# Kernel optimization log

Measured on AMD Instinct MI355X. Metric: run time of the kernel, lower is better.

The kernel has to match this reference:

```python
import jax, jax.numpy as jnp
import numpy as np

DT = 0.1
THRESH = 0.01


def setup_inputs() -> dict:
    key = jax.random.key(0)
    ks = jax.random.split(key, 4)
    B, C, H, W = 4, 64, 128, 128
    field = jax.random.normal(ks[0], (B, C, H, W), dtype=jnp.float32)
    # depthwise 3x3 conv weight [C,1,3,3], fan_in = 9
    dw = jax.random.normal(ks[1], (C, 1, 3, 3), dtype=jnp.float32) * (1.0 / 3.0)
    db = jnp.zeros((C,), jnp.float32)
    # 1x1 convs as matrices: w1 [2C, C], w2 [C, 2C]
    w1 = jax.random.normal(ks[2], (2 * C, C), dtype=jnp.float32) * (1.0 / np.sqrt(C))
    b1 = jnp.zeros((2 * C,), jnp.float32)
    w2 = jax.random.normal(ks[3], (C, 2 * C), dtype=jnp.float32) * (1.0 / np.sqrt(2 * C))
    b2 = jnp.zeros((C,), jnp.float32)
    dcoeff = jnp.ones((1,), jnp.float32) * 0.1  # diffusion_coeff init
    return {"field": field, "dw": dw, "db": db, "w1": w1, "b1": b1,
            "w2": w2, "b2": b2, "dcoeff": dcoeff, "max_steps": 50}


def _dynamics(f, dw, db, w1, b1, w2, b2, dcoeff):
    C = f.shape[1]
    diff = jax.lax.conv_general_dilated(
        f, dw, window_strides=(1, 1), padding="SAME",
        feature_group_count=C,
        dimension_numbers=("NCHW", "OIHW", "NCHW")) + db[None, :, None, None]
    h = jax.nn.gelu(jnp.einsum("bchw,oc->bohw", f, w1) + b1[None, :, None, None],
                    approximate=False)
    react = jnp.einsum("bchw,oc->bohw", h, w2) + b2[None, :, None, None]
    return dcoeff[0] * diff + react


def reference(field, dw, db, w1, b1, w2, b2, dcoeff, max_steps):
    def step(carry, _):
        f, done, steps = carry
        deriv = _dynamics(f, dw, db, w1, b1, w2, b2, dcoeff)
        new_f = f + DT * deriv
        change = jnp.mean(jnp.abs(new_f - f))
        f2 = jnp.where(done, f, new_f)          # freeze field once converged
        steps2 = steps + jnp.where(done, 0, 1)  # steps_taken is adaptive
        done2 = done | (change < THRESH)
        return (f2, done2, steps2), None

    init = (field, jnp.asarray(False), jnp.asarray(0, jnp.int32))
    (final_field, _, steps), _ = jax.lax.scan(step, init, None, length=max_steps)
    return final_field, steps
```

## Files before the change

kernel.cpp:

```cpp
#include <hip/hip_runtime.h>
#include <math.h>

#define BATCH 4
#define CCH   64
#define HDIM  128
#define WDIM  128
#define HW    (HDIM * WDIM)
#define NELEM (BATCH * CCH * HW)
#define OCH   128
#define NSTEPS 50
#define NBLK  1024
#define DT 0.1f
#define THRESH 0.01f

typedef short bf16x8 __attribute__((ext_vector_type(8)));
typedef float f32x4  __attribute__((ext_vector_type(4)));

struct Ctl {
    int done;
    int steps;
};

__global__ void init_kernel(Ctl* ctl) {
    ctl->done = 0;
    ctl->steps = 0;
}

__device__ __forceinline__ short f2bf(float x) {
    unsigned u = __float_as_uint(x);
    unsigned r = u + 0x7fff + ((u >> 16) & 1);
    return (short)(r >> 16);
}

__device__ __forceinline__ int pk(float a, float b) {
    return (f2bf(a) & 0xffff) | (((int)f2bf(b)) << 16);
}

__device__ __forceinline__ float bf_lo(int v) { return __int_as_float(v << 16); }
__device__ __forceinline__ float bf_hi(int v) { return __int_as_float(v & 0xffff0000); }

__global__ void prep_kernel(const float* __restrict__ w1,
                            const float* __restrict__ w2,
                            short* __restrict__ w1b, short* __restrict__ w2b) {
    int i = blockIdx.x * blockDim.x + threadIdx.x;
    if (i < OCH * CCH) {
        w1b[i] = f2bf(w1[i]);
        w2b[i] = f2bf(w2[i]);
    }
}

__device__ __forceinline__ float gelu_fast(float x) {
    float u  = x * 0.70710678118654752f;
    float au = fabsf(u);
    float t  = __builtin_amdgcn_rcpf(fmaf(0.3275911f, au, 1.0f));
    float p  = fmaf(1.061405429f, t, -1.453152027f);
    p = fmaf(p, t, 1.421413741f);
    p = fmaf(p, t, -0.284496736f);
    p = fmaf(p, t, 0.254829592f);
    p = p * t;
    float ex = __expf(-au * au);
    float e  = fmaf(-p, ex, 1.0f);
    float er = copysignf(e, x);
    return 0.5f * x * (1.0f + er);
}

__global__ __launch_bounds__(256, 4) void step_kernel(
    const float* __restrict__ fin, float* __restrict__ fout,
    const float* __restrict__ dw, const float* __restrict__ db,
    const short* __restrict__ w1b, const float* __restrict__ b1,
    const short* __restrict__ w2b, const float* __restrict__ b2,
    const float* __restrict__ dcoeff, const Ctl* __restrict__ ctl,
    double* __restrict__ psum)
{
    if (ctl->done) return;

    const int tid  = threadIdx.x;
    const int lane = tid & 63;
    const int w    = tid >> 6;
    const int quad = (lane >> 4);
    const int lp   = lane & 15;
    const int blk  = blockIdx.x;
    const int xcd  = blk & 7;
    const int idx  = blk >> 3;
    const int y    = xcd * 16 + (idx & 15);
    const int b    = (idx >> 4) & 3;
    const int seg  = idx >> 6;
    const int px0  = seg * 64;
    const int fbase = b * CCH * HW + y * WDIM + px0;

    __shared__ int4  sBf4[64 * 8];
    __shared__ int4  sH4 [64 * 16];
    __shared__ float sSeam[384];
    __shared__ float sDw[CCH * 9];
    __shared__ float sDb[CCH];
    __shared__ float wred[4];
    short* sBf = (short*)sBf4;
    short* sH  = (short*)sH4;
    int*   sRi = (int*)sBf4;

    for (int i = tid; i < CCH * 9; i += 256) sDw[i] = dw[i];
    if (tid < CCH) sDb[tid] = db[tid];

    if (tid < 192) {
        #pragma unroll
        for (int k = 0; k < 2; ++k) {
            int e    = tid * 2 + k;
            int row  = e >> 7;
            int side = (e >> 6) & 1;
            int ch   = e & 63;
            int gy   = y - 1 + row;
            int gx   = px0 + (side ? 64 : -1);
            float v  = 0.0f;
            if (gy >= 0 && gy < HDIM && gx >= 0 && gx < WDIM)
                v = fin[b * CCH * HW + ch * HW + gy * WDIM + gx];
            sSeam[e] = v;
        }
    }

    bf16x8 a1[2][2];
    #pragma unroll
    for (int mt = 0; mt < 2; ++mt)
        #pragma unroll
        for (int kk = 0; kk < 2; ++kk)
            a1[mt][kk] = *(const bf16x8*)(w1b + (w * 32 + mt * 16 + lp) * CCH
                                          + kk * 32 + quad * 8);
    f32x4 b1v[2];
    #pragma unroll
    for (int mt = 0; mt < 2; ++mt)
        b1v[mt] = *(const f32x4*)(b1 + w * 32 + mt * 16 + quad * 4);
    f32x4 b2v = *(const f32x4*)(b2 + w * 16 + quad * 4);

    float f[16];
    {
        #pragma unroll
        for (int i = 0; i < 16; ++i)
            f[i] = fin[fbase + (w * 16 + i) * HW + lane];
        int4 v0, v1;
        v0.x = pk(f[0], f[1]);   v0.y = pk(f[2], f[3]);
        v0.z = pk(f[4], f[5]);   v0.w = pk(f[6], f[7]);
        v1.x = pk(f[8], f[9]);   v1.y = pk(f[10], f[11]);
        v1.z = pk(f[12], f[13]); v1.w = pk(f[14], f[15]);
        int g0 = (w * 2)     ^ (lane & 7);
        int g1 = (w * 2 + 1) ^ (lane & 7);
        sBf4[lane * 8 + g0] = v0;
        sBf4[lane * 8 + g1] = v1;
    }
    __syncthreads();

    f32x4 acc1[2][4];
    #pragma unroll
    for (int mt = 0; mt < 2; ++mt)
        #pragma unroll
        for (int nt = 0; nt < 4; ++nt)
            acc1[mt][nt] = (f32x4)0.0f;

    #pragma unroll
    for (int kk = 0; kk < 2; ++kk) {
        #pragma unroll
        for (int nt = 0; nt < 4; ++nt) {
            int px = nt * 16 + lp;
            int g  = kk * 4 + quad;
            bf16x8 bfrag = *(const bf16x8*)(sBf + px * 64 + (g ^ (px & 7)) * 8);
            #pragma unroll
            for (int mt = 0; mt < 2; ++mt)
                acc1[mt][nt] = __builtin_amdgcn_mfma_f32_16x16x32_bf16(
                    a1[mt][kk], bfrag, acc1[mt][nt], 0, 0, 0);
        }
    }

    #pragma unroll
    for (int mt = 0; mt < 2; ++mt) {
        #pragma unroll
        for (int nt = 0; nt < 4; ++nt) {
            int px = nt * 16 + lp;
            float h0 = gelu_fast(acc1[mt][nt][0] + b1v[mt][0]);
            float h1 = gelu_fast(acc1[mt][nt][1] + b1v[mt][1]);
            float h2 = gelu_fast(acc1[mt][nt][2] + b1v[mt][2]);
            float h3 = gelu_fast(acc1[mt][nt][3] + b1v[mt][3]);
            int o0  = w * 32 + mt * 16 + quad * 4;
            int g   = o0 >> 3;
            int sub = o0 & 7;
            int gp  = (g & 8) | ((g ^ (px & 7)) & 7);
            int2 hv; hv.x = pk(h0, h1); hv.y = pk(h2, h3);
            *(int2*)(sH + px * 128 + gp * 8 + sub) = hv;
        }
    }
    __syncthreads();

    bf16x8 a2[4];
    #pragma unroll
    for (int kk = 0; kk < 4; ++kk)
        a2[kk] = *(const bf16x8*)(w2b + (w * 16 + lp) * OCH + kk * 32 + quad * 8);

    f32x4 acc2[4];
    #pragma unroll
    for (int nt = 0; nt < 4; ++nt) acc2[nt] = (f32x4)0.0f;

    #pragma unroll
    for (int kk = 0; kk < 4; ++kk) {
        #pragma unroll
        for (int nt = 0; nt < 4; ++nt) {
            int px = nt * 16 + lp;
            int g  = kk * 4 + quad;
            int gp = (g & 8) | ((g ^ (px & 7)) & 7);
            bf16x8 hfrag = *(const bf16x8*)(sH + px * 128 + gp * 8);
            acc2[nt] = __builtin_amdgcn_mfma_f32_16x16x32_bf16(
                a2[kk], hfrag, acc2[nt], 0, 0, 0);
        }
    }

    float hm[16], hp[16];
    {
        const float* fb = fin + fbase + lane;
        if (y > 0) {
            #pragma unroll
            for (int i = 0; i < 16; ++i) hm[i] = fb[(w * 16 + i) * HW - WDIM];
        } else {
            #pragma unroll
            for (int i = 0; i < 16; ++i) hm[i] = 0.0f;
        }
        if (y < HDIM - 1) {
            #pragma unroll
            for (int i = 0; i < 16; ++i) hp[i] = fb[(w * 16 + i) * HW + WDIM];
        } else {
            #pragma unroll
            for (int i = 0; i < 16; ++i) hp[i] = 0.0f;
        }
    }

    #pragma unroll
    for (int nt = 0; nt < 4; ++nt) {
        int px = nt * 16 + lp;
        sRi[(w * 8 + quad * 2 + 0) * 64 + px]
            = pk(acc2[nt][0] + b2v[0], acc2[nt][1] + b2v[1]);
        sRi[(w * 8 + quad * 2 + 1) * 64 + px]
            = pk(acc2[nt][2] + b2v[2], acc2[nt][3] + b2v[3]);
    }
    __syncthreads();

    float react[16];
    #pragma unroll
    for (int ii = 0; ii < 8; ++ii) {
        int v = sRi[(w * 8 + ii) * 64 + lane];
        react[2 * ii]     = bf_lo(v);
        react[2 * ii + 1] = bf_hi(v);
    }

    const float dc = dcoeff[0];
    float csum = 0.0f;

    #pragma unroll
    for (int i = 0; i < 16; ++i) {
        const int c = w * 16 + i;
        const float* wk = sDw + c * 9;
        float vm = hm[i], vc = f[i], vp = hp[i];
        float lm = __shfl_up(vm, 1),  lc = __shfl_up(vc, 1),  lq = __shfl_up(vp, 1);
        float rm = __shfl_down(vm, 1), rc = __shfl_down(vc, 1), rq = __shfl_down(vp, 1);
        lm = (lane == 0)  ? sSeam[0 * 128 + 0 + c]   : lm;
        lc = (lane == 0)  ? sSeam[1 * 128 + 0 + c]   : lc;
        lq = (lane == 0)  ? sSeam[2 * 128 + 0 + c]   : lq;
        rm = (lane == 63) ? sSeam[0 * 128 + 64 + c]  : rm;
        rc = (lane == 63) ? sSeam[1 * 128 + 64 + c]  : rc;
        rq = (lane == 63) ? sSeam[2 * 128 + 64 + c]  : rq;

        float d = sDb[c];
        d = fmaf(wk[0], lm, d); d = fmaf(wk[1], vm, d); d = fmaf(wk[2], rm, d);
        d = fmaf(wk[3], lc, d); d = fmaf(wk[4], vc, d); d = fmaf(wk[5], rc, d);
        d = fmaf(wk[6], lq, d); d = fmaf(wk[7], vp, d); d = fmaf(wk[8], rq, d);

        float nf = vc + DT * (dc * d + react[i]);
        fout[fbase + c * HW + lane] = nf;
        csum += fabsf(nf - vc);
    }

    float v = csum;
    #pragma unroll
    for (int off = 32; off > 0; off >>= 1) v += __shfl_down(v, off, 64);
    if (lane == 0) wred[w] = v;
    __syncthreads();
    if (tid == 0) {
        psum[blk] = (double)wred[0] + (double)wred[1]
                  + (double)wred[2] + (double)wred[3];
    }
}

__global__ __launch_bounds__(256) void finalize_kernel(
    Ctl* __restrict__ ctl, const double* __restrict__ psum)
{
    if (ctl->done) return;
    __shared__ double sd[256];
    int t = threadIdx.x;
    sd[t] = psum[t] + psum[t + 256] + psum[t + 512] + psum[t + 768];
    __syncthreads();
    for (int off = 128; off > 0; off >>= 1) {
        if (t < off) sd[t] += sd[t + off];
        __syncthreads();
    }
    if (t == 0) {
        ctl->steps += 1;
        float change = (float)(sd[0] * (1.0 / (double)NELEM));
        if (change < THRESH) ctl->done = 1;
    }
}

__global__ void output_kernel(const float* __restrict__ bufA,
                              float* __restrict__ out,
                              const Ctl* __restrict__ ctl)
{
    int i = blockIdx.x * blockDim.x + threadIdx.x;
    bool fromA = (((ctl->steps - 1) & 1) == 0);
    if (i < NELEM && fromA) out[i] = bufA[i];
    if (i == 0) out[NELEM] = (float)ctl->steps;
}

extern "C" void kernel_launch(void* const* d_in, const int* in_sizes, int n_in,
                              void* d_out, int out_size, void* d_ws, size_t ws_size,
                              hipStream_t stream)
{
    const float* field  = (const float*)d_in[0];
    const float* dw     = (const float*)d_in[1];
    const float* db     = (const float*)d_in[2];
    const float* w1     = (const float*)d_in[3];
    const float* b1     = (const float*)d_in[4];
    const float* w2     = (const float*)d_in[5];
    const float* b2     = (const float*)d_in[6];
    const float* dcoeff = (const float*)d_in[7];

    float* out = (float*)d_out;

    char* ws = (char*)d_ws;
    float*  bufA = (float*)ws;
    Ctl*    ctl  = (Ctl*)(ws + (size_t)NELEM * 4);
    short*  w1b  = (short*)(ws + (size_t)NELEM * 4 + 256);
    short*  w2b  = (short*)(ws + (size_t)NELEM * 4 + 256 + 16384);
    double* psum = (double*)(ws + (size_t)NELEM * 4 + 256 + 32768);

    init_kernel<<<1, 1, 0, stream>>>(ctl);
    prep_kernel<<<(OCH * CCH + 255) / 256, 256, 0, stream>>>(w1, w2, w1b, w2b);

    float* bufs[2] = { bufA, out };
    const float* fin = field;
    for (int s = 1; s <= NSTEPS; ++s) {
        float* fout = bufs[(s - 1) & 1];
        step_kernel<<<NBLK, 256, 0, stream>>>(
            fin, fout, dw, db, w1b, b1, w2b, b2, dcoeff, ctl, psum);
        finalize_kernel<<<1, 256, 0, stream>>>(ctl, psum);
        fin = fout;
    }

    output_kernel<<<(NELEM + 255) / 256, 256, 0, stream>>>(bufA, out, ctl);
}
```

Measured before the change: 1.234 ms.

## Fold convergence reduction into step kernel and drop finalize launches

Each step block now reduces the previous step's 1024 partial sums itself, using ping-pong psum buffers, to decide convergence. This removes the separate single-block finalize kernel and its launch and serialization gap at every step. The steps counter is written by block 0. Once converged, blocks forward their old partial sum and exit early. The vertical-neighbor loads are also hoisted before the second GEMM so their latency overlaps it, at the cost of every block redundantly reading 8KB of partials and more register pressure.

```diff
diff --git a/kernel.cpp b/kernel.cpp
--- a/kernel.cpp
+++ b/kernel.cpp
@@ -16,14 +16,13 @@
 typedef short bf16x8 __attribute__((ext_vector_type(8)));
 typedef float f32x4  __attribute__((ext_vector_type(4)));
 
-struct Ctl {
-    int done;
-    int steps;
-};
-
-__global__ void init_kernel(Ctl* ctl) {
-    ctl->done = 0;
-    ctl->steps = 0;
+__global__ void init_kernel(double* p0, double* p1, int* stepsvar) {
+    int i = blockIdx.x * blockDim.x + threadIdx.x;
+    if (i < NBLK) {
+        p0[i] = (i == 0) ? 1.0e9 : 0.0;
+        p1[i] = 0.0;
+    }
+    if (i == 0) *stepsvar = 0;
 }
 
 __device__ __forceinline__ short f2bf(float x) {
@@ -69,11 +68,10 @@
     const float* __restrict__ dw, const float* __restrict__ db,
     const short* __restrict__ w1b, const float* __restrict__ b1,
     const short* __restrict__ w2b, const float* __restrict__ b2,
-    const float* __restrict__ dcoeff, const Ctl* __restrict__ ctl,
-    double* __restrict__ psum)
+    const float* __restrict__ dcoeff,
+    const double* __restrict__ pin, double* __restrict__ pout,
+    int* __restrict__ stepsvar, int sidx)
 {
-    if (ctl->done) return;
-
     const int tid  = threadIdx.x;
     const int lane = tid & 63;
     const int w    = tid >> 6;
@@ -88,15 +86,21 @@
     const int px0  = seg * 64;
     const int fbase = b * CCH * HW + y * WDIM + px0;
 
-    __shared__ int4  sBf4[64 * 8];
-    __shared__ int4  sH4 [64 * 16];
-    __shared__ float sSeam[384];
-    __shared__ float sDw[CCH * 9];
-    __shared__ float sDb[CCH];
-    __shared__ float wred[4];
+    __shared__ int4   sBf4[64 * 8];
+    __shared__ int4   sH4 [64 * 16];
+    __shared__ float  sSeam[384];
+    __shared__ float  sDw[CCH * 9];
+    __shared__ float  sDb[CCH];
+    __shared__ double sdred[4];
+    __shared__ float  wred[4];
     short* sBf = (short*)sBf4;
     short* sH  = (short*)sH4;
     int*   sRi = (int*)sBf4;
+
+    double ds = pin[tid] + pin[tid + 256] + pin[tid + 512] + pin[tid + 768];
+    #pragma unroll
+    for (int off = 32; off > 0; off >>= 1) ds += __shfl_down(ds, off, 64);
+    if (lane == 0) sdred[w] = ds;
 
     for (int i = tid; i < CCH * 9; i += 256) sDw[i] = dw[i];
     if (tid < CCH) sDb[tid] = db[tid];
@@ -146,6 +150,15 @@
         sBf4[lane * 8 + g1] = v1;
     }
     __syncthreads();
+
+    {
+        double tot = sdred[0] + sdred[1] + sdred[2] + sdred[3];
+        if ((float)(tot * (1.0 / (double)NELEM)) < THRESH) {
+            if (tid == 0) pout[blk] = pin[blk];
+            return;
+        }
+    }
+    if (blk == 0 && tid == 0) *stepsvar = sidx + 1;
 
     f32x4 acc1[2][4];
     #pragma unroll
@@ -185,6 +198,25 @@
             *(int2*)(sH + px * 128 + gp * 8 + sub) = hv;
         }
     }
+
+    float hm[16], hp[16];
+    {
+        const float* fb = fin + fbase + lane;
+        if (y > 0) {
+            #pragma unroll
+            for (int i = 0; i < 16; ++i) hm[i] = fb[(w * 16 + i) * HW - WDIM];
+        } else {
+            #pragma unroll
+            for (int i = 0; i < 16; ++i) hm[i] = 0.0f;
+        }
+        if (y < HDIM - 1) {
+            #pragma unroll
+            for (int i = 0; i < 16; ++i) hp[i] = fb[(w * 16 + i) * HW + WDIM];
+        } else {
+            #pragma unroll
+            for (int i = 0; i < 16; ++i) hp[i] = 0.0f;
+        }
+    }
     __syncthreads();
 
     bf16x8 a2[4];
@@ -206,25 +238,6 @@
             bf16x8 hfrag = *(const bf16x8*)(sH + px * 128 + gp * 8);
             acc2[nt] = __builtin_amdgcn_mfma_f32_16x16x32_bf16(
                 a2[kk], hfrag, acc2[nt], 0, 0, 0);
-        }
-    }
-
-    float hm[16], hp[16];
-    {
-        const float* fb = fin + fbase + lane;
-        if (y > 0) {
-            #pragma unroll
-            for (int i = 0; i < 16; ++i) hm[i] = fb[(w * 16 + i) * HW - WDIM];
-        } else {
-            #pragma unroll
-            for (int i = 0; i < 16; ++i) hm[i] = 0.0f;
-        }
-        if (y < HDIM - 1) {
-            #pragma unroll
-            for (int i = 0; i < 16; ++i) hp[i] = fb[(w * 16 + i) * HW + WDIM];
-        } else {
-            #pragma unroll
-            for (int i = 0; i < 16; ++i) hp[i] = 0.0f;
         }
     }
 
@@ -279,38 +292,20 @@
     if (lane == 0) wred[w] = v;
     __syncthreads();
     if (tid == 0) {
-        psum[blk] = (double)wred[0] + (double)wred[1]
+        pout[blk] = (double)wred[0] + (double)wred[1]
                   + (double)wred[2] + (double)wred[3];
-    }
-}
-
-__global__ __launch_bounds__(256) void finalize_kernel(
-    Ctl* __restrict__ ctl, const double* __restrict__ psum)
-{
-    if (ctl->done) return;
-    __shared__ double sd[256];
-    int t = threadIdx.x;
-    sd[t] = psum[t] + psum[t + 256] + psum[t + 512] + psum[t + 768];
-    __syncthreads();
-    for (int off = 128; off > 0; off >>= 1) {
-        if (t < off) sd[t] += sd[t + off];
-        __syncthreads();
-    }
-    if (t == 0) {
-        ctl->steps += 1;
-        float change = (float)(sd[0] * (1.0 / (double)NELEM));
-        if (change < THRESH) ctl->done = 1;
     }
 }
 
 __global__ void output_kernel(const float* __restrict__ bufA,
                               float* __restrict__ out,
-                              const Ctl* __restrict__ ctl)
+                              const int* __restrict__ stepsvar)
 {
     int i = blockIdx.x * blockDim.x + threadIdx.x;
-    bool fromA = (((ctl->steps - 1) & 1) == 0);
+    int K = *stepsvar;
+    bool fromA = (((K - 1) & 1) == 0);
     if (i < NELEM && fromA) out[i] = bufA[i];
-    if (i == 0) out[NELEM] = (float)ctl->steps;
+    if (i == 0) out[NELEM] = (float)K;
 }
 
 extern "C" void kernel_launch(void* const* d_in, const int* in_sizes, int n_in,
@@ -330,23 +325,25 @@
 
     char* ws = (char*)d_ws;
     float*  bufA = (float*)ws;
-    Ctl*    ctl  = (Ctl*)(ws + (size_t)NELEM * 4);
     short*  w1b  = (short*)(ws + (size_t)NELEM * 4 + 256);
     short*  w2b  = (short*)(ws + (size_t)NELEM * 4 + 256 + 16384);
-    double* psum = (double*)(ws + (size_t)NELEM * 4 + 256 + 32768);
-
-    init_kernel<<<1, 1, 0, stream>>>(ctl);
+    double* P0   = (double*)(ws + (size_t)NELEM * 4 + 256 + 32768);
+    double* P1   = P0 + NBLK;
+    int* stepsvar = (int*)(P1 + NBLK);
+
+    init_kernel<<<4, 256, 0, stream>>>(P0, P1, stepsvar);
     prep_kernel<<<(OCH * CCH + 255) / 256, 256, 0, stream>>>(w1, w2, w1b, w2b);
 
-    float* bufs[2] = { bufA, out };
+    float*  bufs[2]  = { bufA, out };
+    double* psums[2] = { P0, P1 };
     const float* fin = field;
     for (int s = 1; s <= NSTEPS; ++s) {
         float* fout = bufs[(s - 1) & 1];
         step_kernel<<<NBLK, 256, 0, stream>>>(
-            fin, fout, dw, db, w1b, b1, w2b, b2, dcoeff, ctl, psum);
-        finalize_kernel<<<1, 256, 0, stream>>>(ctl, psum);
+            fin, fout, dw, db, w1b, b1, w2b, b2, dcoeff,
+            psums[(s - 1) & 1], psums[s & 1], stepsvar, s - 1);
         fin = fout;
     }
 
-    output_kernel<<<(NELEM + 255) / 256, 256, 0, stream>>>(bufA, out, ctl);
-}
+    output_kernel<<<(NELEM + 255) / 256, 256, 0, stream>>>(bufA, out, stepsvar);
+}
```

After: 1.115 ms. 1.11x faster.
